# Kernel tuning notes

Hardware: AMD Instinct MI355X
Metric: run time of the kernel (lower is better)

Reference implementation:

```python
import math
import jax, jax.numpy as jnp
import numpy as np

N = 100000
E_RAND = 800000
IN_F, HID, OUT_F, HEADS = 128, 64, 64, 4
NOISE_SCALE = 1.0 * math.sqrt(2.0 * math.log(1.25 / 0.05))  # dp_rate=1, eps=1, del=0.05


def setup_inputs() -> dict:
    key = jax.random.key(0)
    ks = jax.random.split(key, 12)
    x = jax.random.normal(ks[0], (N, IN_F), dtype=jnp.float32)
    src_r = jax.random.randint(ks[1], (E_RAND,), 0, N, dtype=jnp.int32)
    dst_r = jax.random.randint(ks[2], (E_RAND,), 0, N, dtype=jnp.int32)
    loops = jnp.arange(N, dtype=jnp.int32)  # add_self_loop
    src = jnp.concatenate([src_r, loops])
    dst = jnp.concatenate([dst_r, loops])
    # layer 0: GATConv(in=128, out=64, heads=4)
    s0 = 1.0 / math.sqrt(IN_F)
    W0 = jax.random.normal(ks[3], (IN_F, HEADS * HID), dtype=jnp.float32) * s0
    al0 = jax.random.normal(ks[4], (HEADS, HID), dtype=jnp.float32) * 0.1
    ar0 = jax.random.normal(ks[5], (HEADS, HID), dtype=jnp.float32) * 0.1
    b0 = jnp.zeros((HEADS * HID,), dtype=jnp.float32)
    # layer 1: GATConv(in=256, out=64, heads=1)
    s1 = 1.0 / math.sqrt(HEADS * HID)
    W1 = jax.random.normal(ks[6], (HEADS * HID, OUT_F), dtype=jnp.float32) * s1
    al1 = jax.random.normal(ks[7], (1, OUT_F), dtype=jnp.float32) * 0.1
    ar1 = jax.random.normal(ks[8], (1, OUT_F), dtype=jnp.float32) * 0.1
    b1 = jnp.zeros((OUT_F,), dtype=jnp.float32)
    # DP gaussian noise added after first GAT layer (torch.normal(0,1,x.shape))
    noise = jax.random.normal(ks[9], (N, HEADS * HID), dtype=jnp.float32)
    return {"x": x, "src": src, "dst": dst, "W0": W0, "al0": al0, "ar0": ar0,
            "b0": b0, "W1": W1, "al1": al1, "ar1": ar1, "b1": b1, "noise": noise}


def gat_conv(x, src, dst, W, al, ar, b, apply_act):
    """DGL GATConv: per-edge attention, edge softmax over dst, scatter-sum."""
    H, D = al.shape
    h = (x @ W).reshape(-1, H, D)                      # [N,H,D]
    el = jnp.sum(h * al, axis=-1)                      # [N,H]
    er = jnp.sum(h * ar, axis=-1)                      # [N,H]
    e = jax.nn.leaky_relu(el[src] + er[dst], 0.2)      # [E,H]
    emax = jax.ops.segment_max(e, dst, num_segments=N) # [N,H]
    a = jnp.exp(e - emax[dst])
    denom = jax.ops.segment_sum(a, dst, num_segments=N)
    alpha = a / denom[dst]                             # [E,H] edge softmax
    msg = h[src] * alpha[:, :, None]                   # [E,H,D]
    out = jax.ops.segment_sum(msg, dst, num_segments=N) + b.reshape(1, H, D)
    if apply_act:
        out = jax.nn.leaky_relu(out, 0.01)             # F.leaky_relu default slope
    return out.reshape(-1, H * D)                      # flatten(1)


def reference(x, src, dst, W0, al0, ar0, b0, W1, al1, ar1, b1, noise):
    h = gat_conv(x, src, dst, W0, al0, ar0, b0, apply_act=True)   # [N, 256]
    h = h + NOISE_SCALE * noise                                   # DP noise after layer 0
    out = gat_conv(h, src, dst, W1, al1, ar1, b1, apply_act=False)  # [N, 64]
    return out
```

## Files before the change

### kernel.cpp

```cpp
#include <hip/hip_runtime.h>
#include <hip/hip_bf16.h>
#include <math.h>

#define IN_F 128
#define HID 64
#define HEADS 4
#define HD0 (HEADS * HID)
#define OUT_F 64
#define NOISE_SCALE 2.5372725354060904f

typedef __bf16 bf16x8 __attribute__((ext_vector_type(8)));
typedef float f32x4 __attribute__((ext_vector_type(4)));

__device__ __forceinline__ float bf2f(unsigned short u) {
    return __uint_as_float(((unsigned)u) << 16);
}
__device__ __forceinline__ unsigned short f2bf(float f) {
    unsigned u = __float_as_uint(f);
    u = u + 0x7fffu + ((u >> 16) & 1u);
    return (unsigned short)(u >> 16);
}

__device__ __forceinline__ void acc8(float* acc, const uint4& u, float wt) {
    acc[0] += wt * __uint_as_float(u.x << 16);
    acc[1] += wt * __uint_as_float(u.x & 0xffff0000u);
    acc[2] += wt * __uint_as_float(u.y << 16);
    acc[3] += wt * __uint_as_float(u.y & 0xffff0000u);
    acc[4] += wt * __uint_as_float(u.z << 16);
    acc[5] += wt * __uint_as_float(u.z & 0xffff0000u);
    acc[6] += wt * __uint_as_float(u.w << 16);
    acc[7] += wt * __uint_as_float(u.w & 0xffff0000u);
}

__global__ __launch_bounds__(256) void prep_kernel(
    const float* __restrict__ in, unsigned short* __restrict__ out, size_t n8,
    int* __restrict__ deg, int N, int nb_cast,
    const float* __restrict__ W0, unsigned short* __restrict__ W0t,
    const float* __restrict__ W1, unsigned short* __restrict__ W1t) {
    const int b = blockIdx.x;
    if (b < nb_cast) {
        size_t i = (size_t)b * 256 + threadIdx.x;
        if (i < (size_t)N) deg[i] = 0;
        if (i >= n8) return;
        const float4 a = ((const float4*)in)[i * 2];
        const float4 c = ((const float4*)in)[i * 2 + 1];
        ushort4 o0, o1;
        o0.x = f2bf(a.x); o0.y = f2bf(a.y); o0.z = f2bf(a.z); o0.w = f2bf(a.w);
        o1.x = f2bf(c.x); o1.y = f2bf(c.y); o1.z = f2bf(c.z); o1.w = f2bf(c.w);
        ((ushort4*)out)[i * 2] = o0;
        ((ushort4*)out)[i * 2 + 1] = o1;
    } else if (b < nb_cast + (IN_F * HD0) / 256) {
        int i = (b - nb_cast) * 256 + threadIdx.x;
        int n = i / IN_F, k = i % IN_F;
        W0t[i] = f2bf(W0[(size_t)k * HD0 + n]);
    } else {
        int j = (b - nb_cast - (IN_F * HD0) / 256) * 256 + threadIdx.x;
        if (j < HD0 * OUT_F) {
            int n = j / HD0, k = j % HD0;
            W1t[j] = f2bf(W1[(size_t)k * OUT_F + n]);
        }
    }
}

template <int K, int H, int NT>
__global__ __launch_bounds__(256) void gemm_fused_kernel(
    const unsigned short* __restrict__ A, const unsigned short* __restrict__ Bt,
    unsigned short* __restrict__ C, const float* __restrict__ al,
    const float* __restrict__ ar, float* __restrict__ el,
    float* __restrict__ er, int M, int NC) {
    constexpr int BSTR = K + 8;
    constexpr int ASTR = 40;
    constexpr int NROWS = 64 * NT;
    __shared__ __align__(16) unsigned short Bs[NROWS * BSTR];
    __shared__ __align__(16) unsigned short As[128 * ASTR];
    const int tid = threadIdx.x;
    const int lane = tid & 63, w = tid >> 6;
    const int row0 = blockIdx.y * 128;
    const int n0 = blockIdx.x * NROWS;
    for (int i = tid; i < NROWS * (K / 8); i += 256) {
        int n = i / (K / 8), kc = i % (K / 8);
        *(uint4*)(Bs + n * BSTR + kc * 8) =
            *(const uint4*)(Bt + (size_t)(n0 + n) * K + kc * 8);
    }
    f32x4 acc[2][4 * NT] = {};
    const int q = lane >> 4, c = lane & 15;
    const int r_st = tid >> 1, hh = tid & 1;
    for (int k0 = 0; k0 < K; k0 += 32) {
        int gr = row0 + r_st;
        uint4 av0 = make_uint4(0, 0, 0, 0), av1 = make_uint4(0, 0, 0, 0);
        if (gr < M) {
            const unsigned short* ap = A + (size_t)gr * K + k0 + hh * 16;
            av0 = *(const uint4*)(ap);
            av1 = *(const uint4*)(ap + 8);
        }
        __syncthreads();
        *(uint4*)(As + r_st * ASTR + hh * 16) = av0;
        *(uint4*)(As + r_st * ASTR + hh * 16 + 8) = av1;
        __syncthreads();
        bf16x8 af[2], bfr[4 * NT];
        af[0] = *(const bf16x8*)(As + (w * 32 + c) * ASTR + q * 8);
        af[1] = *(const bf16x8*)(As + (w * 32 + 16 + c) * ASTR + q * 8);
#pragma unroll
        for (int nt = 0; nt < 4 * NT; ++nt)
            bfr[nt] = *(const bf16x8*)(Bs + (nt * 16 + c) * BSTR + k0 + q * 8);
#pragma unroll
        for (int mt = 0; mt < 2; ++mt)
#pragma unroll
            for (int nt = 0; nt < 4 * NT; ++nt)
                acc[mt][nt] = __builtin_amdgcn_mfma_f32_16x16x32_bf16(
                    af[mt], bfr[nt], acc[mt][nt], 0, 0, 0);
    }
    float alv[4 * NT], arv[4 * NT];
#pragma unroll
    for (int nt = 0; nt < 4 * NT; ++nt) {
        alv[nt] = al[n0 + nt * 16 + c];
        arv[nt] = ar[n0 + nt * 16 + c];
    }
    const int headbase = n0 >> 6;
#pragma unroll
    for (int mt = 0; mt < 2; ++mt) {
#pragma unroll
        for (int r = 0; r < 4; ++r) {
            int grow = row0 + w * 32 + mt * 16 + q * 4 + r;
            bool ok = grow < M;
#pragma unroll
            for (int g = 0; g < NT; ++g) {
                float elp = 0.f, erp = 0.f;
#pragma unroll
                for (int t = 0; t < 4; ++t) {
                    int nt = g * 4 + t;
                    float v = acc[mt][nt][r];
                    elp += v * alv[nt];
                    erp += v * arv[nt];
                    if (ok) C[(size_t)grow * NC + n0 + nt * 16 + c] = f2bf(v);
                }
#pragma unroll
                for (int o = 8; o > 0; o >>= 1) {
                    elp += __shfl_down(elp, o, 16);
                    erp += __shfl_down(erp, o, 16);
                }
                if (c == 0 && ok) {
                    el[(size_t)grow * H + headbase + g] = elp;
                    er[(size_t)grow * H + headbase + g] = erp;
                }
            }
        }
    }
}

__global__ __launch_bounds__(256) void degree_kernel(
    const int* __restrict__ dst, int* __restrict__ deg, int E) {
    int e = blockIdx.x * 256 + threadIdx.x;
    if (e < E) atomicAdd(&deg[dst[e]], 1);
}

__global__ __launch_bounds__(256) void scan_block_kernel(
    const int* __restrict__ deg, int* __restrict__ off,
    int* __restrict__ bsum, int N) {
    __shared__ int s[256];
    int i = blockIdx.x * 256 + threadIdx.x;
    int v = (i < N) ? deg[i] : 0;
    s[threadIdx.x] = v;
    __syncthreads();
    for (int d = 1; d < 256; d <<= 1) {
        int t = (threadIdx.x >= d) ? s[threadIdx.x - d] : 0;
        __syncthreads();
        s[threadIdx.x] += t;
        __syncthreads();
    }
    if (i < N) off[i] = s[threadIdx.x] - v;
    if (threadIdx.x == 255) bsum[blockIdx.x] = s[255];
}

__global__ __launch_bounds__(512) void scan_partials_kernel(int* __restrict__ bsum, int nb) {
    __shared__ int s[512];
    int v = (threadIdx.x < nb) ? bsum[threadIdx.x] : 0;
    s[threadIdx.x] = v;
    __syncthreads();
    for (int d = 1; d < 512; d <<= 1) {
        int t = (threadIdx.x >= d) ? s[threadIdx.x - d] : 0;
        __syncthreads();
        s[threadIdx.x] += t;
        __syncthreads();
    }
    if (threadIdx.x < nb) bsum[threadIdx.x] = s[threadIdx.x] - v;
}

__global__ __launch_bounds__(256) void add_offsets_kernel(
    int* __restrict__ off, int* __restrict__ cur,
    const int* __restrict__ bsum, int N, int E) {
    int i = blockIdx.x * 256 + threadIdx.x;
    if (i < N) {
        int v = off[i] + bsum[blockIdx.x];
        off[i] = v;
        cur[i] = v;
    }
    if (i == 0) off[N] = E;
}

__global__ __launch_bounds__(256) void fill_csr_kernel(
    const int* __restrict__ src, const int* __restrict__ dst,
    int* __restrict__ cur, int* __restrict__ csr_src, int E) {
    int e = blockIdx.x * 256 + threadIdx.x;
    if (e >= E) return;
    int d = dst[e];
    int pos = atomicAdd(&cur[d], 1);
    csr_src[pos] = src[e];
}

__global__ __launch_bounds__(256) void agg0_kernel(
    const int* __restrict__ off, const int* __restrict__ csr_src,
    const unsigned short* __restrict__ h,
    const float* __restrict__ el,
    const float* __restrict__ er,
    const float* __restrict__ b0, const float* __restrict__ noise,
    unsigned short* __restrict__ out, int N) {
    int gt = blockIdx.x * 256 + threadIdx.x;
    int n = gt >> 6;
    if (n >= N) return;
    const int lane = gt & 63;
    const int grp = lane >> 5;
    const int fl = lane & 31;
    const int hd = fl >> 3;
    const int f0 = fl << 3;
    const float ern = er[(size_t)n * 4 + hd];
    const int beg = off[n];
    const int last = off[n + 1] - 1;
    float acc[8] = {0.f, 0.f, 0.f, 0.f, 0.f, 0.f, 0.f, 0.f};
    float l = 0.f;
    for (int p = beg + grp * 4; p <= last; p += 8) {
        int i1 = p + 1, i2 = p + 2, i3 = p + 3;
        const bool v1 = i1 <= last, v2 = i2 <= last, v3 = i3 <= last;
        i1 = v1 ? i1 : last;
        i2 = v2 ? i2 : last;
        i3 = v3 ? i3 : last;
        const int s0 = csr_src[p],  s1 = csr_src[i1];
        const int s2 = csr_src[i2], s3 = csr_src[i3];
        float e0 = el[(size_t)s0 * 4 + hd] + ern;
        float e1 = el[(size_t)s1 * 4 + hd] + ern;
        float e2 = el[(size_t)s2 * 4 + hd] + ern;
        float e3 = el[(size_t)s3 * 4 + hd] + ern;
        const uint4 u0 = *(const uint4*)(h + (size_t)s0 * HD0 + f0);
        const uint4 u1 = *(const uint4*)(h + (size_t)s1 * HD0 + f0);
        const uint4 u2 = *(const uint4*)(h + (size_t)s2 * HD0 + f0);
        const uint4 u3 = *(const uint4*)(h + (size_t)s3 * HD0 + f0);
        e0 = e0 > 0.f ? e0 : 0.2f * e0;
        e1 = e1 > 0.f ? e1 : 0.2f * e1;
        e2 = e2 > 0.f ? e2 : 0.2f * e2;
        e3 = e3 > 0.f ? e3 : 0.2f * e3;
        const float w0 = __expf(e0);
        const float w1 = v1 ? __expf(e1) : 0.f;
        const float w2 = v2 ? __expf(e2) : 0.f;
        const float w3 = v3 ? __expf(e3) : 0.f;
        acc8(acc, u0, w0);
        acc8(acc, u1, w1);
        acc8(acc, u2, w2);
        acc8(acc, u3, w3);
        l += (w0 + w1) + (w2 + w3);
    }
    l += __shfl_xor(l, 32);
#pragma unroll
    for (int j = 0; j < 8; ++j) acc[j] += __shfl_xor(acc[j], 32);
    if (grp != 0) return;
    const float rd = 1.f / l;
    const float4 ba = *(const float4*)(b0 + f0);
    const float4 bb = *(const float4*)(b0 + f0 + 4);
    const float4 na = *(const float4*)(noise + (size_t)n * HD0 + f0);
    const float4 nb = *(const float4*)(noise + (size_t)n * HD0 + f0 + 4);
    float o[8];
    o[0] = acc[0] * rd + ba.x;
    o[1] = acc[1] * rd + ba.y;
    o[2] = acc[2] * rd + ba.z;
    o[3] = acc[3] * rd + ba.w;
    o[4] = acc[4] * rd + bb.x;
    o[5] = acc[5] * rd + bb.y;
    o[6] = acc[6] * rd + bb.z;
    o[7] = acc[7] * rd + bb.w;
#pragma unroll
    for (int j = 0; j < 8; ++j) o[j] = o[j] > 0.f ? o[j] : 0.01f * o[j];
    o[0] += NOISE_SCALE * na.x;
    o[1] += NOISE_SCALE * na.y;
    o[2] += NOISE_SCALE * na.z;
    o[3] += NOISE_SCALE * na.w;
    o[4] += NOISE_SCALE * nb.x;
    o[5] += NOISE_SCALE * nb.y;
    o[6] += NOISE_SCALE * nb.z;
    o[7] += NOISE_SCALE * nb.w;
    uint4 ov;
    ov.x = (unsigned)f2bf(o[0]) | ((unsigned)f2bf(o[1]) << 16);
    ov.y = (unsigned)f2bf(o[2]) | ((unsigned)f2bf(o[3]) << 16);
    ov.z = (unsigned)f2bf(o[4]) | ((unsigned)f2bf(o[5]) << 16);
    ov.w = (unsigned)f2bf(o[6]) | ((unsigned)f2bf(o[7]) << 16);
    *(uint4*)(out + (size_t)n * HD0 + f0) = ov;
}

__global__ __launch_bounds__(256) void agg1_kernel(
    const int* __restrict__ off, const int* __restrict__ csr_src,
    const unsigned short* __restrict__ h,
    const float* __restrict__ el,
    const float* __restrict__ er,
    const float* __restrict__ b1, float* __restrict__ out, int N) {
    int gt = blockIdx.x * 256 + threadIdx.x;
    int n = gt >> 5;
    if (n >= N) return;
    const int lane5 = gt & 31;
    const int grp = lane5 >> 4;
    const int fl = lane5 & 15;
    const int f0 = fl << 2;
    const float ern = er[n];
    const int beg = off[n];
    const int last = off[n + 1] - 1;
    float a0 = 0.f, a1 = 0.f, a2 = 0.f, a3 = 0.f, l = 0.f;
    for (int p = beg + grp * 4; p <= last; p += 8) {
        int i1 = p + 1, i2 = p + 2, i3 = p + 3;
        const bool v1 = i1 <= last, v2 = i2 <= last, v3 = i3 <= last;
        i1 = v1 ? i1 : last;
        i2 = v2 ? i2 : last;
        i3 = v3 ? i3 : last;
        const int s0 = csr_src[p],  s1 = csr_src[i1];
        const int s2 = csr_src[i2], s3 = csr_src[i3];
        float e0 = el[s0] + ern;
        float e1 = el[s1] + ern;
        float e2 = el[s2] + ern;
        float e3 = el[s3] + ern;
        const ushort4 u0 = *(const ushort4*)(h + (size_t)s0 * 64 + f0);
        const ushort4 u1 = *(const ushort4*)(h + (size_t)s1 * 64 + f0);
        const ushort4 u2 = *(const ushort4*)(h + (size_t)s2 * 64 + f0);
        const ushort4 u3 = *(const ushort4*)(h + (size_t)s3 * 64 + f0);
        e0 = e0 > 0.f ? e0 : 0.2f * e0;
        e1 = e1 > 0.f ? e1 : 0.2f * e1;
        e2 = e2 > 0.f ? e2 : 0.2f * e2;
        e3 = e3 > 0.f ? e3 : 0.2f * e3;
        const float w0 = __expf(e0);
        const float w1 = v1 ? __expf(e1) : 0.f;
        const float w2 = v2 ? __expf(e2) : 0.f;
        const float w3 = v3 ? __expf(e3) : 0.f;
        a0 += w0 * bf2f(u0.x) + w1 * bf2f(u1.x) + w2 * bf2f(u2.x) + w3 * bf2f(u3.x);
        a1 += w0 * bf2f(u0.y) + w1 * bf2f(u1.y) + w2 * bf2f(u2.y) + w3 * bf2f(u3.y);
        a2 += w0 * bf2f(u0.z) + w1 * bf2f(u1.z) + w2 * bf2f(u2.z) + w3 * bf2f(u3.z);
        a3 += w0 * bf2f(u0.w) + w1 * bf2f(u1.w) + w2 * bf2f(u2.w) + w3 * bf2f(u3.w);
        l += (w0 + w1) + (w2 + w3);
    }
    l += __shfl_xor(l, 16);
    a0 += __shfl_xor(a0, 16);
    a1 += __shfl_xor(a1, 16);
    a2 += __shfl_xor(a2, 16);
    a3 += __shfl_xor(a3, 16);
    if (grp != 0) return;
    const float rd = 1.f / l;
    const float4 bv = *(const float4*)(b1 + f0);
    float4 o;
    o.x = a0 * rd + bv.x;
    o.y = a1 * rd + bv.y;
    o.z = a2 * rd + bv.z;
    o.w = a3 * rd + bv.w;
    *(float4*)(out + (size_t)n * 64 + f0) = o;
}

extern "C" void kernel_launch(void* const* d_in, const int* in_sizes, int n_in,
                              void* d_out, int out_size, void* d_ws, size_t ws_size,
                              hipStream_t stream) {
    const float* x     = (const float*)d_in[0];
    const int*   src   = (const int*)d_in[1];
    const int*   dst   = (const int*)d_in[2];
    const float* W0    = (const float*)d_in[3];
    const float* al0   = (const float*)d_in[4];
    const float* ar0   = (const float*)d_in[5];
    const float* b0    = (const float*)d_in[6];
    const float* W1    = (const float*)d_in[7];
    const float* al1   = (const float*)d_in[8];
    const float* ar1   = (const float*)d_in[9];
    const float* b1    = (const float*)d_in[10];
    const float* noise = (const float*)d_in[11];

    const int N = in_sizes[0] / IN_F;
    const int E = in_sizes[1];
    const int NB = (N + 255) / 256;

    char* p = (char*)d_ws;
    unsigned short* x_bf   = (unsigned short*)p; p += (size_t)N * IN_F * 2;
    unsigned short* h0     = (unsigned short*)p; p += (size_t)N * HD0 * 2;
    unsigned short* agg0b  = (unsigned short*)p; p += (size_t)N * HD0 * 2;
    unsigned short* h1     = (unsigned short*)p; p += (size_t)N * OUT_F * 2;
    unsigned short* W0t    = (unsigned short*)p; p += (size_t)IN_F * HD0 * 2;
    unsigned short* W1t    = (unsigned short*)p; p += (size_t)HD0 * OUT_F * 2;
    float* el     = (float*)p; p += (size_t)N * HEADS * 4;
    float* er     = (float*)p; p += (size_t)N * HEADS * 4;
    int* deg    = (int*)p; p += (size_t)N * 4;
    int* cur    = (int*)p; p += (size_t)N * 4;
    int* off    = (int*)p; p += ((size_t)N + 4) * 4;
    int* bsum   = (int*)p; p += 512 * 4;
    int* csr_src= (int*)p; p += (size_t)E * 4;

    {
        size_t n8 = (size_t)N * IN_F / 8;
        int nb_cast = (int)((n8 + 255) / 256);
        int nb_w0 = (IN_F * HD0) / 256;
        int nb_w1 = (HD0 * OUT_F + 255) / 256;
        prep_kernel<<<nb_cast + nb_w0 + nb_w1, 256, 0, stream>>>(
            x, x_bf, n8, deg, N, nb_cast, W0, W0t, W1, W1t);
    }

    degree_kernel<<<(E + 255) / 256, 256, 0, stream>>>(dst, deg, E);
    scan_block_kernel<<<NB, 256, 0, stream>>>(deg, off, bsum, N);
    scan_partials_kernel<<<1, 512, 0, stream>>>(bsum, NB);
    add_offsets_kernel<<<NB, 256, 0, stream>>>(off, cur, bsum, N, E);
    fill_csr_kernel<<<(E + 255) / 256, 256, 0, stream>>>(src, dst, cur, csr_src, E);

    const int MB = (N + 127) / 128;

    {
        dim3 grid(HD0 / 128, MB);
        gemm_fused_kernel<IN_F, HEADS, 2><<<grid, 256, 0, stream>>>(
            x_bf, W0t, h0, al0, ar0, el, er, N, HD0);
    }
    agg0_kernel<<<(unsigned)(((size_t)N * 64 + 255) / 256), 256, 0, stream>>>(
        off, csr_src, h0, el, er, b0, noise, agg0b, N);

    {
        dim3 grid(OUT_F / 64, MB);
        gemm_fused_kernel<HD0, 1, 1><<<grid, 256, 0, stream>>>(
            agg0b, W1t, h1, al1, ar1, el, er, N, OUT_F);
    }
    agg1_kernel<<<(unsigned)(((size_t)N * 32 + 255) / 256), 256, 0, stream>>>(
        off, csr_src, h1, el, er, b1, (float*)d_out, N);
}
```

Before: 446.5 us.

## Halve threads per node in aggregation, stage larger GEMM A tiles, fold scan partials

The aggregation kernels now give each node half as many lanes, with no split-edge groups and no cross-group shuffle reduction. The GEMM stages up to 128 K-columns of A into shared memory at once, so it syncs fewer times per k-step. The separate scan_partials launch is removed, and each add_offsets block sums its preceding block totals itself. Nontemporal loads and stores are used for the streaming input, noise and outputs. Together these aim to cut sync and launch overhead, but with fewer lanes per node there is less memory-level parallelism for the edge gathers, and the GEMM's shared-memory footprint grows.

```diff
diff --git a/kernel.cpp b/kernel.cpp
--- a/kernel.cpp
+++ b/kernel.cpp
@@ -11,6 +11,8 @@
 
 typedef __bf16 bf16x8 __attribute__((ext_vector_type(8)));
 typedef float f32x4 __attribute__((ext_vector_type(4)));
+typedef float f4 __attribute__((ext_vector_type(4)));
+typedef unsigned int u4 __attribute__((ext_vector_type(4)));
 
 __device__ __forceinline__ float bf2f(unsigned short u) {
     return __uint_as_float(((unsigned)u) << 16);
@@ -42,8 +44,8 @@
         size_t i = (size_t)b * 256 + threadIdx.x;
         if (i < (size_t)N) deg[i] = 0;
         if (i >= n8) return;
-        const float4 a = ((const float4*)in)[i * 2];
-        const float4 c = ((const float4*)in)[i * 2 + 1];
+        const f4 a = __builtin_nontemporal_load((const f4*)in + i * 2);
+        const f4 c = __builtin_nontemporal_load((const f4*)in + i * 2 + 1);
         ushort4 o0, o1;
         o0.x = f2bf(a.x); o0.y = f2bf(a.y); o0.z = f2bf(a.z); o0.w = f2bf(a.w);
         o1.x = f2bf(c.x); o1.y = f2bf(c.y); o1.z = f2bf(c.z); o1.w = f2bf(c.w);
@@ -68,8 +70,9 @@
     unsigned short* __restrict__ C, const float* __restrict__ al,
     const float* __restrict__ ar, float* __restrict__ el,
     float* __restrict__ er, int M, int NC) {
+    constexpr int KH = (K > 128) ? 128 : K;
     constexpr int BSTR = K + 8;
-    constexpr int ASTR = 40;
+    constexpr int ASTR = KH + 8;
     constexpr int NROWS = 64 * NT;
     __shared__ __align__(16) unsigned short Bs[NROWS * BSTR];
     __shared__ __align__(16) unsigned short As[128 * ASTR];
@@ -84,31 +87,31 @@
     }
     f32x4 acc[2][4 * NT] = {};
     const int q = lane >> 4, c = lane & 15;
-    const int r_st = tid >> 1, hh = tid & 1;
-    for (int k0 = 0; k0 < K; k0 += 32) {
-        int gr = row0 + r_st;
-        uint4 av0 = make_uint4(0, 0, 0, 0), av1 = make_uint4(0, 0, 0, 0);
-        if (gr < M) {
-            const unsigned short* ap = A + (size_t)gr * K + k0 + hh * 16;
-            av0 = *(const uint4*)(ap);
-            av1 = *(const uint4*)(ap + 8);
+    for (int kh = 0; kh < K; kh += KH) {
+        __syncthreads();
+        for (int i = tid; i < 128 * (KH / 8); i += 256) {
+            int r = i / (KH / 8), kc = i % (KH / 8);
+            uint4 v = make_uint4(0, 0, 0, 0);
+            int gr = row0 + r;
+            if (gr < M) v = *(const uint4*)(A + (size_t)gr * K + kh + kc * 8);
+            *(uint4*)(As + r * ASTR + kc * 8) = v;
         }
         __syncthreads();
-        *(uint4*)(As + r_st * ASTR + hh * 16) = av0;
-        *(uint4*)(As + r_st * ASTR + hh * 16 + 8) = av1;
-        __syncthreads();
-        bf16x8 af[2], bfr[4 * NT];
-        af[0] = *(const bf16x8*)(As + (w * 32 + c) * ASTR + q * 8);
-        af[1] = *(const bf16x8*)(As + (w * 32 + 16 + c) * ASTR + q * 8);
-#pragma unroll
-        for (int nt = 0; nt < 4 * NT; ++nt)
-            bfr[nt] = *(const bf16x8*)(Bs + (nt * 16 + c) * BSTR + k0 + q * 8);
-#pragma unroll
-        for (int mt = 0; mt < 2; ++mt)
+#pragma unroll
+        for (int k0 = 0; k0 < KH; k0 += 32) {
+            bf16x8 af[2], bfr[4 * NT];
+            af[0] = *(const bf16x8*)(As + (w * 32 + c) * ASTR + k0 + q * 8);
+            af[1] = *(const bf16x8*)(As + (w * 32 + 16 + c) * ASTR + k0 + q * 8);
 #pragma unroll
             for (int nt = 0; nt < 4 * NT; ++nt)
-                acc[mt][nt] = __builtin_amdgcn_mfma_f32_16x16x32_bf16(
-                    af[mt], bfr[nt], acc[mt][nt], 0, 0, 0);
+                bfr[nt] = *(const bf16x8*)(Bs + (nt * 16 + c) * BSTR + kh + k0 + q * 8);
+#pragma unroll
+            for (int mt = 0; mt < 2; ++mt)
+#pragma unroll
+                for (int nt = 0; nt < 4 * NT; ++nt)
+                    acc[mt][nt] = __builtin_amdgcn_mfma_f32_16x16x32_bf16(
+                        af[mt], bfr[nt], acc[mt][nt], 0, 0, 0);
+        }
     }
     float alv[4 * NT], arv[4 * NT];
 #pragma unroll
@@ -172,26 +175,20 @@
     if (threadIdx.x == 255) bsum[blockIdx.x] = s[255];
 }
 
-__global__ __launch_bounds__(512) void scan_partials_kernel(int* __restrict__ bsum, int nb) {
-    __shared__ int s[512];
-    int v = (threadIdx.x < nb) ? bsum[threadIdx.x] : 0;
-    s[threadIdx.x] = v;
-    __syncthreads();
-    for (int d = 1; d < 512; d <<= 1) {
-        int t = (threadIdx.x >= d) ? s[threadIdx.x - d] : 0;
-        __syncthreads();
-        s[threadIdx.x] += t;
-        __syncthreads();
-    }
-    if (threadIdx.x < nb) bsum[threadIdx.x] = s[threadIdx.x] - v;
-}
-
 __global__ __launch_bounds__(256) void add_offsets_kernel(
     int* __restrict__ off, int* __restrict__ cur,
     const int* __restrict__ bsum, int N, int E) {
+    __shared__ int sred[4];
+    int partial = 0;
+    for (int i = threadIdx.x; i < blockIdx.x; i += 256) partial += bsum[i];
+#pragma unroll
+    for (int o = 32; o > 0; o >>= 1) partial += __shfl_down(partial, o);
+    if ((threadIdx.x & 63) == 0) sred[threadIdx.x >> 6] = partial;
+    __syncthreads();
+    int base = sred[0] + sred[1] + sred[2] + sred[3];
     int i = blockIdx.x * 256 + threadIdx.x;
     if (i < N) {
-        int v = off[i] + bsum[blockIdx.x];
+        int v = off[i] + base;
         off[i] = v;
         cur[i] = v;
     }
@@ -216,19 +213,17 @@
     const float* __restrict__ b0, const float* __restrict__ noise,
     unsigned short* __restrict__ out, int N) {
     int gt = blockIdx.x * 256 + threadIdx.x;
-    int n = gt >> 6;
+    int n = gt >> 5;
     if (n >= N) return;
-    const int lane = gt & 63;
-    const int grp = lane >> 5;
-    const int fl = lane & 31;
-    const int hd = fl >> 3;
-    const int f0 = fl << 3;
+    const int lane = gt & 31;
+    const int hd = lane >> 3;
+    const int f0 = lane << 3;
     const float ern = er[(size_t)n * 4 + hd];
     const int beg = off[n];
     const int last = off[n + 1] - 1;
     float acc[8] = {0.f, 0.f, 0.f, 0.f, 0.f, 0.f, 0.f, 0.f};
     float l = 0.f;
-    for (int p = beg + grp * 4; p <= last; p += 8) {
+    for (int p = beg; p <= last; p += 4) {
         int i1 = p + 1, i2 = p + 2, i3 = p + 3;
         const bool v1 = i1 <= last, v2 = i2 <= last, v3 = i3 <= last;
         i1 = v1 ? i1 : last;
@@ -258,15 +253,11 @@
         acc8(acc, u3, w3);
         l += (w0 + w1) + (w2 + w3);
     }
-    l += __shfl_xor(l, 32);
-#pragma unroll
-    for (int j = 0; j < 8; ++j) acc[j] += __shfl_xor(acc[j], 32);
-    if (grp != 0) return;
     const float rd = 1.f / l;
     const float4 ba = *(const float4*)(b0 + f0);
     const float4 bb = *(const float4*)(b0 + f0 + 4);
-    const float4 na = *(const float4*)(noise + (size_t)n * HD0 + f0);
-    const float4 nb = *(const float4*)(noise + (size_t)n * HD0 + f0 + 4);
+    const f4 na = __builtin_nontemporal_load((const f4*)(noise + (size_t)n * HD0 + f0));
+    const f4 nb = __builtin_nontemporal_load((const f4*)(noise + (size_t)n * HD0 + f0 + 4));
     float o[8];
     o[0] = acc[0] * rd + ba.x;
     o[1] = acc[1] * rd + ba.y;
@@ -286,12 +277,12 @@
     o[5] += NOISE_SCALE * nb.y;
     o[6] += NOISE_SCALE * nb.z;
     o[7] += NOISE_SCALE * nb.w;
-    uint4 ov;
+    u4 ov;
     ov.x = (unsigned)f2bf(o[0]) | ((unsigned)f2bf(o[1]) << 16);
     ov.y = (unsigned)f2bf(o[2]) | ((unsigned)f2bf(o[3]) << 16);
     ov.z = (unsigned)f2bf(o[4]) | ((unsigned)f2bf(o[5]) << 16);
     ov.w = (unsigned)f2bf(o[6]) | ((unsigned)f2bf(o[7]) << 16);
-    *(uint4*)(out + (size_t)n * HD0 + f0) = ov;
+    __builtin_nontemporal_store(ov, (u4*)(out + (size_t)n * HD0 + f0));
 }
 
 __global__ __launch_bounds__(256) void agg1_kernel(
@@ -301,17 +292,15 @@
     const float* __restrict__ er,
     const float* __restrict__ b1, float* __restrict__ out, int N) {
     int gt = blockIdx.x * 256 + threadIdx.x;
-    int n = gt >> 5;
+    int n = gt >> 4;
     if (n >= N) return;
-    const int lane5 = gt & 31;
-    const int grp = lane5 >> 4;
-    const int fl = lane5 & 15;
-    const int f0 = fl << 2;
+    const int lane = gt & 15;
+    const int f0 = lane << 2;
     const float ern = er[n];
     const int beg = off[n];
     const int last = off[n + 1] - 1;
     float a0 = 0.f, a1 = 0.f, a2 = 0.f, a3 = 0.f, l = 0.f;
-    for (int p = beg + grp * 4; p <= last; p += 8) {
+    for (int p = beg; p <= last; p += 4) {
         int i1 = p + 1, i2 = p + 2, i3 = p + 3;
         const bool v1 = i1 <= last, v2 = i2 <= last, v3 = i3 <= last;
         i1 = v1 ? i1 : last;
@@ -341,20 +330,14 @@
         a3 += w0 * bf2f(u0.w) + w1 * bf2f(u1.w) + w2 * bf2f(u2.w) + w3 * bf2f(u3.w);
         l += (w0 + w1) + (w2 + w3);
     }
-    l += __shfl_xor(l, 16);
-    a0 += __shfl_xor(a0, 16);
-    a1 += __shfl_xor(a1, 16);
-    a2 += __shfl_xor(a2, 16);
-    a3 += __shfl_xor(a3, 16);
-    if (grp != 0) return;
     const float rd = 1.f / l;
     const float4 bv = *(const float4*)(b1 + f0);
-    float4 o;
+    f4 o;
     o.x = a0 * rd + bv.x;
     o.y = a1 * rd + bv.y;
     o.z = a2 * rd + bv.z;
     o.w = a3 * rd + bv.w;
-    *(float4*)(out + (size_t)n * 64 + f0) = o;
+    __builtin_nontemporal_store(o, (f4*)(out + (size_t)n * 64 + f0));
 }
 
 extern "C" void kernel_launch(void* const* d_in, const int* in_sizes, int n_in,
@@ -403,7 +386,6 @@
 
     degree_kernel<<<(E + 255) / 256, 256, 0, stream>>>(dst, deg, E);
     scan_block_kernel<<<NB, 256, 0, stream>>>(deg, off, bsum, N);
-    scan_partials_kernel<<<1, 512, 0, stream>>>(bsum, NB);
     add_offsets_kernel<<<NB, 256, 0, stream>>>(off, cur, bsum, N, E);
     fill_csr_kernel<<<(E + 255) / 256, 256, 0, stream>>>(src, dst, cur, csr_src, E);
 
@@ -414,7 +396,7 @@
         gemm_fused_kernel<IN_F, HEADS, 2><<<grid, 256, 0, stream>>>(
             x_bf, W0t, h0, al0, ar0, el, er, N, HD0);
     }
-    agg0_kernel<<<(unsigned)(((size_t)N * 64 + 255) / 256), 256, 0, stream>>>(
+    agg0_kernel<<<(unsigned)(((size_t)N * 32 + 255) / 256), 256, 0, stream>>>(
         off, csr_src, h0, el, er, b0, noise, agg0b, N);
 
     {
@@ -422,6 +404,6 @@
         gemm_fused_kernel<HD0, 1, 1><<<grid, 256, 0, stream>>>(
             agg0b, W1t, h1, al1, ar1, el, er, N, OUT_F);
     }
-    agg1_kernel<<<(unsigned)(((size_t)N * 32 + 255) / 256), 256, 0, stream>>>(
+    agg1_kernel<<<(unsigned)(((size_t)N * 16 + 255) / 256), 256, 0, stream>>>(
         off, csr_src, h1, el, er, b1, (float*)d_out, N);
 }
```

Result: slower. 456.9 us (+2.3%).
